# Kernel tuning notes

Measured on AMD Instinct MI355X. Metric: run time of the kernel, lower is better.

Reference implementation:

```python
import jax, jax.numpy as jnp
import numpy as np

N_NODES = 50000
N_EDGES = 800000
HIDDEN = 256
N_LAYERS = 3
N_PAIRS = 4096


def setup_inputs() -> dict:
    key = jax.random.key(0)
    ks = jax.random.split(key, 10)
    s = 1.0 / np.sqrt(HIDDEN)
    x = jax.random.normal(ks[0], (N_NODES, HIDDEN), dtype=jnp.float32)
    f0_w = jax.random.normal(ks[1], (N_LAYERS, HIDDEN, HIDDEN), dtype=jnp.float32) * s
    f0_b = jax.random.normal(ks[2], (N_LAYERS, HIDDEN), dtype=jnp.float32) * s
    f1_w = jax.random.normal(ks[3], (N_LAYERS, HIDDEN, HIDDEN), dtype=jnp.float32) * s
    f1_b = jax.random.normal(ks[4], (N_LAYERS, HIDDEN), dtype=jnp.float32) * s
    conv_w = jax.random.normal(ks[5], (N_LAYERS, HIDDEN, HIDDEN), dtype=jnp.float32) * s
    conv_b = jax.random.normal(ks[6], (N_LAYERS, HIDDEN), dtype=jnp.float32) * s
    edge_src = jax.random.randint(ks[7], (N_EDGES,), 0, N_NODES, dtype=jnp.int64 if jax.config.jax_enable_x64 else jnp.int32)
    edge_dst = jax.random.randint(ks[8], (N_EDGES,), 0, N_NODES, dtype=edge_src.dtype)
    pos = jax.random.randint(ks[9], (N_PAIRS, 2), 0, N_NODES, dtype=edge_src.dtype)
    return {"x": x, "f0_w": f0_w, "f0_b": f0_b, "f1_w": f1_w, "f1_b": f1_b,
            "conv_w": conv_w, "conv_b": conv_b,
            "edge_src": edge_src, "edge_dst": edge_dst, "pos": pos}


def reference(x, f0_w, f0_b, f1_w, f1_b, conv_w, conv_b, edge_src, edge_dst, pos):
    # Faithful translation of FLabelingNet.forward:
    #   for each layer: x0 = f0(x); x0[idx] = f1(x[idx]); x = conv(x0, adj)
    #   return x[pos]
    n = x.shape[0]
    idx = pos.reshape(-1)  # (2M,) labeled node indices
    for i in range(f0_w.shape[0]):
        x0 = x @ f0_w[i] + f0_b[i]                       # (N, F) elementwise linear
        lbl = x[idx] @ f1_w[i] + f1_b[i]                 # (2M, F) transform of labeled rows
        x0 = x0.at[idx].set(lbl)                         # scatter-overwrite selected rows
        h = x0 @ conv_w[i] + conv_b[i]                   # node-wise linear of the conv
        # sparse adjacency message passing: out[v] = sum_{(u,v) in E} h[u]
        x = jax.ops.segment_sum(h[edge_src], edge_dst, num_segments=n)
    return x[pos]  # (M, 2, F)
```

## Files before the change

### kernel.cpp

```cpp
#include <hip/hip_runtime.h>
#include <hip/hip_bf16.h>

#define N_NODES 50000
#define N_EDGES 800000
#define HIDDEN  256
#define N_LAYERS 3
#define N_PAIRS 4096
#define N_LABEL 8192
#define NPAD    50176
#define SCAN_BLOCKS (NPAD / 256)
#define WSZ (HIDDEN * HIDDEN)
#define NSTEP (HIDDEN / 32)
#define NBUCKET 196
#define EDGE_BLOCKS 196

#define NROWPAD (N_NODES + 1)
#define SLICE_ELEMS ((size_t)NROWPAD * 32)
#define SEG_CHUNKS ((N_NODES + 63) / 64)

typedef __bf16 bf16x8 __attribute__((ext_vector_type(8)));
typedef float  f32x4  __attribute__((ext_vector_type(4)));
typedef float  f32x2  __attribute__((ext_vector_type(2)));

__device__ __forceinline__ void load_lds16(const void* g, void* l) {
    __builtin_amdgcn_global_load_lds(
        (const __attribute__((address_space(1))) void*)g,
        (__attribute__((address_space(3))) void*)l, 16, 0, 0);
}

__device__ __forceinline__ void acc8(const uint4 w, f32x2* a) {
    a[0] += (f32x2){__uint_as_float(w.x << 16), __uint_as_float(w.x & 0xffff0000u)};
    a[1] += (f32x2){__uint_as_float(w.y << 16), __uint_as_float(w.y & 0xffff0000u)};
    a[2] += (f32x2){__uint_as_float(w.z << 16), __uint_as_float(w.z & 0xffff0000u)};
    a[3] += (f32x2){__uint_as_float(w.w << 16), __uint_as_float(w.w & 0xffff0000u)};
}

template <bool DEG_BIAS>
__global__ __launch_bounds__(256) void mfma_gemm_fused(
    const __bf16* __restrict__ A,
    const __bf16* __restrict__ Wt0, const __bf16* __restrict__ Wt1,
    const float* __restrict__ bD0, const float* __restrict__ bD1,
    const float* __restrict__ bC0, const float* __restrict__ bC1,
    __bf16* __restrict__ Cout,
    const int* __restrict__ idx,
    const int* __restrict__ degv,
    const int* __restrict__ flags,
    int M)
{
    const int role = blockIdx.z;
    const int bx = blockIdx.x, by = blockIdx.y;
    if (role == 1 && bx >= N_LABEL / 64) return;

    const __bf16* Wt = role ? Wt1 : Wt0;
    const float*  bD = role ? bD1 : bD0;
    const float*  bC = role ? bC1 : bC0;

    __shared__ __bf16 As[3 * 64 * 32];
    __shared__ __bf16 Bs[3 * 128 * 32];
    __shared__ int s_idx[64];

    const int t    = threadIdx.x;
    const int lane = t & 63;
    const int wave = t >> 6;
    const int m0   = bx * 64;
    const int n0   = by * 128;

    if (role == 1) {
        if (t < 64) s_idx[t] = idx[m0 + t];
        __syncthreads();
    }

    const int arow  = t >> 2;
    const int acol8 = (t & 3) * 8;
    int anode;
    if (role == 1) {
        anode = s_idx[arow];
    } else {
        const int rg = m0 + arow;
        anode = (rg < M) ? rg : (M - 1);
    }
    const __bf16* aptr = A + (size_t)anode * HIDDEN + acol8;

    const __bf16* bptr[2];
    #pragma unroll
    for (int r = 0; r < 2; ++r) {
        const int c = r * 256 + t;
        bptr[r] = Wt + (size_t)(n0 + (c >> 2)) * HIDDEN + (c & 3) * 8;
    }

    f32x4 acc[8];
    #pragma unroll
    for (int i = 0; i < 8; ++i) acc[i] = (f32x4){0.f, 0.f, 0.f, 0.f};

    const int wm   = wave * 16;
    const int fm   = lane & 15;
    const int quad = lane >> 4;

    const __bf16* bp0 = bptr[0];
    const __bf16* bp1 = bptr[1];
    #define STAGE_F(SB, K0)                                                    \
        { load_lds16(aptr + (K0), (void*)(As + (SB) * 2048 + (size_t)t * 8));  \
          load_lds16(bp0 + (K0),  (void*)(Bs + (SB) * 4096 + (size_t)t * 8));  \
          load_lds16(bp1 + (K0),  (void*)(Bs + (SB) * 4096 + (size_t)(256 + t) * 8)); }

    STAGE_F(0, 0)
    STAGE_F(1, 32)
    asm volatile("s_waitcnt vmcnt(3)" ::: "memory");
    __builtin_amdgcn_sched_barrier(0);
    __builtin_amdgcn_s_barrier();

    #pragma unroll
    for (int step = 0; step < NSTEP; ++step) {
        const int cur = step % 3;
        if (step + 2 < NSTEP) {
            const int nb = (step + 2) % 3;
            STAGE_F(nb, (step + 2) * 32)
        }
        const bf16x8 af = *(const bf16x8*)(As + cur * 2048 + (wm + fm) * 32 + quad * 8);
        bf16x8 bfr[8];
        #pragma unroll
        for (int nt = 0; nt < 8; ++nt)
            bfr[nt] = *(const bf16x8*)(Bs + cur * 4096 + (nt * 16 + fm) * 32 + quad * 8);
        #pragma unroll
        for (int nt = 0; nt < 8; ++nt)
            acc[nt] = __builtin_amdgcn_mfma_f32_16x16x32_bf16(
                af, bfr[nt], acc[nt], 0, 0, 0);
        if (step + 2 < NSTEP) asm volatile("s_waitcnt vmcnt(3)" ::: "memory");
        else                  asm volatile("s_waitcnt vmcnt(0)" ::: "memory");
        __builtin_amdgcn_sched_barrier(0);
        __builtin_amdgcn_s_barrier();
    }
    #undef STAGE_F

    float bd[8], bc[8];
    #pragma unroll
    for (int nt = 0; nt < 8; ++nt) {
        const int col = n0 + nt * 16 + fm;
        bd[nt] = DEG_BIAS ? bD[col] : 0.f;
        bc[nt] = bC[col];
    }

    #pragma unroll
    for (int rg = 0; rg < 4; ++rg) {
        const int rloc = wm + quad * 4 + rg;
        int orow;
        if (role == 1) {
            orow = s_idx[rloc];
        } else {
            orow = m0 + rloc;
            if (orow >= M) continue;
            if (flags[orow]) continue;
        }
        float bscale = 0.f;
        if constexpr (DEG_BIAS)
            bscale = (float)degv[orow];
        #pragma unroll
        for (int nt = 0; nt < 8; ++nt) {
            const int cb = n0 + nt * 16;
            float v = acc[nt][rg];
            if constexpr (DEG_BIAS) v += bscale * bd[nt];
            v += bc[nt];
            Cout[(size_t)(cb >> 5) * SLICE_ELEMS + (size_t)orow * 32
                 + (cb & 31) + fm] = (__bf16)v;
        }
    }
}

template <bool GATHER_A, bool DEG_BIAS, bool DEG_VIA_IDX, bool OUT_BF16, bool PROD_BATCH>
__global__ __launch_bounds__(256) void mfma_gemm(
    const __bf16* __restrict__ A_in,
    const __bf16* __restrict__ Wt_in,
    const float* __restrict__ biasD,
    void* __restrict__ Cout_in,
    const int* __restrict__ idx,
    const int* __restrict__ degv,
    int M)
{
    const __bf16* A  = A_in;
    const __bf16* Wt = Wt_in;
    void* Cout = Cout_in;
    if constexpr (PROD_BATCH) {
        const int z = blockIdx.z;
        A    = A_in  + (size_t)(3 * (1 + (z >> 1)) + (z & 1)) * WSZ;
        Wt   = Wt_in + (size_t)(z >> 1) * WSZ;
        Cout = (void*)((__bf16*)Cout_in + (size_t)z * WSZ);
    }

    __shared__ __bf16 As[3 * 64 * 32];
    __shared__ __bf16 Bs[3 * 128 * 32];
    __shared__ int s_idx[64];

    const int t    = threadIdx.x;
    const int lane = t & 63;
    const int wave = t >> 6;
    const int m0   = blockIdx.x * 64;
    const int n0   = blockIdx.y * 128;

    if constexpr (GATHER_A || DEG_VIA_IDX) {
        if (t < 64) s_idx[t] = idx[m0 + t];
        __syncthreads();
    }

    const int arow  = t >> 2;
    const int acol8 = (t & 3) * 8;
    int anode;
    if constexpr (GATHER_A) {
        anode = s_idx[arow];
    } else {
        const int rg = m0 + arow;
        anode = (rg < M) ? rg : (M - 1);
    }
    const __bf16* aptr = A + (size_t)anode * HIDDEN + acol8;

    const __bf16* bptr[2];
    #pragma unroll
    for (int r = 0; r < 2; ++r) {
        const int c = r * 256 + t;
        bptr[r] = Wt + (size_t)(n0 + (c >> 2)) * HIDDEN + (c & 3) * 8;
    }

    f32x4 acc[8];
    #pragma unroll
    for (int i = 0; i < 8; ++i) acc[i] = (f32x4){0.f, 0.f, 0.f, 0.f};

    const int wm   = wave * 16;
    const int fm   = lane & 15;
    const int quad = lane >> 4;

    const __bf16* bp0 = bptr[0];
    const __bf16* bp1 = bptr[1];
    #define STAGE_P(SB, K0)                                                    \
        { load_lds16(aptr + (K0), (void*)(As + (SB) * 2048 + (size_t)t * 8));  \
          load_lds16(bp0 + (K0),  (void*)(Bs + (SB) * 4096 + (size_t)t * 8));  \
          load_lds16(bp1 + (K0),  (void*)(Bs + (SB) * 4096 + (size_t)(256 + t) * 8)); }

    STAGE_P(0, 0)
    STAGE_P(1, 32)
    asm volatile("s_waitcnt vmcnt(3)" ::: "memory");
    __builtin_amdgcn_sched_barrier(0);
    __builtin_amdgcn_s_barrier();

    #pragma unroll
    for (int step = 0; step < NSTEP; ++step) {
        const int cur = step % 3;
        if (step + 2 < NSTEP) {
            const int nb = (step + 2) % 3;
            STAGE_P(nb, (step + 2) * 32)
        }
        const bf16x8 af = *(const bf16x8*)(As + cur * 2048 + (wm + fm) * 32 + quad * 8);
        bf16x8 bfr[8];
        #pragma unroll
        for (int nt = 0; nt < 8; ++nt)
            bfr[nt] = *(const bf16x8*)(Bs + cur * 4096 + (nt * 16 + fm) * 32 + quad * 8);
        #pragma unroll
        for (int nt = 0; nt < 8; ++nt)
            acc[nt] = __builtin_amdgcn_mfma_f32_16x16x32_bf16(
                af, bfr[nt], acc[nt], 0, 0, 0);
        if (step + 2 < NSTEP) asm volatile("s_waitcnt vmcnt(3)" ::: "memory");
        else                  asm volatile("s_waitcnt vmcnt(0)" ::: "memory");
        __builtin_amdgcn_sched_barrier(0);
        __builtin_amdgcn_s_barrier();
    }
    #undef STAGE_P

    float bd[8];
    #pragma unroll
    for (int nt = 0; nt < 8; ++nt)
        bd[nt] = DEG_BIAS ? biasD[n0 + nt * 16 + fm] : 0.f;

    #pragma unroll
    for (int rg = 0; rg < 4; ++rg) {
        const int rloc = wm + quad * 4 + rg;
        const int orow = m0 + rloc;
        if (!PROD_BATCH && orow >= M) continue;
        int dnode = orow;
        if constexpr (GATHER_A || DEG_VIA_IDX) dnode = s_idx[rloc];
        float bscale = 0.f;
        if constexpr (DEG_BIAS)
            bscale = (float)degv[dnode];
        #pragma unroll
        for (int nt = 0; nt < 8; ++nt) {
            const int col = n0 + nt * 16 + fm;
            float v = acc[nt][rg];
            if constexpr (DEG_BIAS) v += bscale * bd[nt];
            if constexpr (OUT_BF16)
                ((__bf16*)Cout)[(size_t)orow * HIDDEN + col] = (__bf16)v;
            else
                ((float*)Cout)[(size_t)orow * HIDDEN + col] = v;
        }
    }
}

__global__ __launch_bounds__(256) void wconv_kernel(
    const float* __restrict__ f0_w, const float* __restrict__ f1_w,
    const float* __restrict__ conv_w, const float* __restrict__ conv_b,
    __bf16* __restrict__ wt_all, __bf16* __restrict__ cw_nt,
    float* __restrict__ q,
    const int* __restrict__ edge_dst, const int* __restrict__ pos,
    int* __restrict__ blkbucket, int* __restrict__ flags,
    __bf16* __restrict__ x0b,
    const float* __restrict__ x32, __bf16* __restrict__ xb16)
{
    const int z = blockIdx.z;
    const int tx = threadIdx.x, ty = threadIdx.y;
    const int tt = ty * 32 + tx;

    if (z >= 16) {
        const int c = (z - 16) * 64 + blockIdx.x * 8 + blockIdx.y;
        const size_t base = ((size_t)c * 256 + tt) * 8;
        if (base < (size_t)N_NODES * HIDDEN) {
            const float4 u0 = *(const float4*)(x32 + base);
            const float4 u1 = *(const float4*)(x32 + base + 4);
            bf16x8 w = {(__bf16)u0.x, (__bf16)u0.y, (__bf16)u0.z, (__bf16)u0.w,
                        (__bf16)u1.x, (__bf16)u1.y, (__bf16)u1.z, (__bf16)u1.w};
            *(bf16x8*)(xb16 + base) = w;
        }
        return;
    }
    if (z >= 12) {
        __shared__ int lhist[256];
        const int blk = (z - 12) * 64 + blockIdx.x * 8 + blockIdx.y;
        if (blk >= EDGE_BLOCKS) return;
        if (blk == 0 && tt < 256) {
            const int sl = tt >> 5, c = tt & 31;
            x0b[(size_t)sl * SLICE_ELEMS + (size_t)N_NODES * 32 + c] = (__bf16)0.f;
        }
        lhist[tt] = 0;
        __syncthreads();
        const int e0 = blk * 4096;
        #pragma unroll
        for (int j = 0; j < 16; ++j) {
            const int e = e0 + j * 256 + tt;
            if (e < N_EDGES) atomicAdd(&lhist[edge_dst[e] >> 8], 1);
            if (e < N_LABEL) flags[pos[e]] = 1;
        }
        __syncthreads();
        if (tt < NBUCKET) blkbucket[blk * 256 + tt] = lhist[tt];
        return;
    }

    const int kx = blockIdx.x * 32, nx = blockIdx.y * 32;

    if (z < 9) {
        const int layer = z / 3, which = z % 3;
        const float* W = ((which == 0) ? f0_w : (which == 1) ? f1_w : conv_w)
                         + (size_t)layer * WSZ;
        __bf16* T = wt_all + (size_t)z * WSZ;

        __shared__ float tile[32][33];
        for (int i = ty; i < 32; i += 8)
            tile[i][tx] = W[(size_t)(kx + i) * HIDDEN + nx + tx];
        __syncthreads();
        for (int i = ty; i < 32; i += 8)
            T[(size_t)(nx + i) * HIDDEN + kx + tx] = (__bf16)tile[tx][i];
    } else if (z < 11) {
        const int layer = z - 9;
        const float* W = conv_w + (size_t)layer * WSZ;
        __bf16* T = cw_nt + (size_t)layer * WSZ;
        for (int i = ty; i < 32; i += 8)
            T[(size_t)(kx + i) * HIDDEN + nx + tx] =
                (__bf16)W[(size_t)(kx + i) * HIDDEN + nx + tx];
    } else {
        if (blockIdx.x >= 4 || blockIdx.y != 0) return;
        const int zq = blockIdx.x;
        const int l = zq >> 1, branch = zq & 1;
        const float* cb = conv_b + (size_t)l * HIDDEN;
        const float* W  = (branch ? f1_w : f0_w) + (size_t)(l + 1) * WSZ;
        const int n = tt;
        float s = 0.f;
        #pragma unroll 4
        for (int k = 0; k < HIDDEN; ++k)
            s += cb[k] * W[(size_t)k * HIDDEN + n];
        q[(size_t)zq * HIDDEN + n] = s;
    }
}

__device__ __forceinline__ int block_incl_scan(int v, int* s, int t)
{
    s[t] = v; __syncthreads();
    #pragma unroll
    for (int off = 1; off < 256; off <<= 1) {
        int add = (t >= off) ? s[t - off] : 0;
        __syncthreads();
        s[t] += add;
        __syncthreads();
    }
    return s[t];
}

__global__ __launch_bounds__(256) void k1b_kernel(
    const int* __restrict__ blkbucket, int* __restrict__ blkbase,
    int* __restrict__ bucket_base, int* __restrict__ bucket_size)
{
    __shared__ int s[256];
    const int t = threadIdx.x;
    int sum = 0;
    if (t < NBUCKET) {
        for (int blk = 0; blk < EDGE_BLOCKS; ++blk) {
            blkbase[blk * 256 + t] = sum;
            sum += blkbucket[blk * 256 + t];
        }
    }
    const int incl = block_incl_scan(sum, s, t);
    const int bb = incl - sum;
    if (t < NBUCKET) {
        bucket_base[t] = bb;
        bucket_size[t] = sum;
        for (int blk = 0; blk < EDGE_BLOCKS; ++blk)
            blkbase[blk * 256 + t] += bb;
    }
}

__global__ __launch_bounds__(256) void k1c_kernel(
    const int* __restrict__ esrc, const int* __restrict__ edst,
    const int* __restrict__ blkbase, unsigned int* __restrict__ bucket_buf)
{
    __shared__ int cur[256];
    const int blk = blockIdx.x;
    const int t = threadIdx.x;
    cur[t] = (t < NBUCKET) ? blkbase[blk * 256 + t] : 0;
    __syncthreads();
    const int e0 = blk * 4096;
    #pragma unroll
    for (int j = 0; j < 16; ++j) {
        const int e = e0 + j * 256 + t;
        if (e < N_EDGES) {
            const int d = edst[e];
            const int p = atomicAdd(&cur[d >> 8], 1);
            bucket_buf[p] = (unsigned int)esrc[e] | ((unsigned int)(d & 255) << 16);
        }
    }
}

__global__ __launch_bounds__(256) void k2a_kernel(
    const unsigned int* __restrict__ bucket_buf,
    const int* __restrict__ bucket_base, const int* __restrict__ bucket_size,
    int* __restrict__ counts, int* __restrict__ offs_local,
    int* __restrict__ bsum)
{
    __shared__ int lcnt[256];
    __shared__ int s[256];
    const int b = blockIdx.x;
    const int t = threadIdx.x;
    lcnt[t] = 0;
    __syncthreads();
    const int bb = bucket_base[b], sz = bucket_size[b];
    for (int j = t; j < sz; j += 256)
        atomicAdd(&lcnt[bucket_buf[bb + j] >> 16], 1);
    __syncthreads();
    const int cnt = lcnt[t];
    counts[b * 256 + t] = cnt;
    const int pv = (cnt + 7) & ~7;
    const int incl = block_incl_scan(pv, s, t);
    offs_local[b * 256 + t] = incl - pv;
    if (t == 255) bsum[b] = incl;
}

__global__ __launch_bounds__(256) void scan2_kernel(
    const int* __restrict__ bsum, int* __restrict__ bbase)
{
    __shared__ int s[256];
    const int t = threadIdx.x;
    const int v = (t < SCAN_BLOCKS) ? bsum[t] : 0;
    int incl = block_incl_scan(v, s, t);
    bbase[t] = incl - v;
}

__global__ __launch_bounds__(256) void k2b_kernel(
    const unsigned int* __restrict__ bucket_buf,
    const int* __restrict__ bucket_base, const int* __restrict__ bucket_size,
    const int* __restrict__ offs_local, const int* __restrict__ bbase,
    int* __restrict__ offs, int* __restrict__ src_sorted)
{
    __shared__ int cur[256];
    const int b = blockIdx.x;
    const int t = threadIdx.x;
    const int off = offs_local[b * 256 + t] + bbase[b];
    offs[b * 256 + t] = off;
    cur[t] = off;
    __syncthreads();
    const int bb = bucket_base[b], sz = bucket_size[b];
    for (int j = t; j < sz; j += 256) {
        const unsigned int u = bucket_buf[bb + j];
        const int p = atomicAdd(&cur[u >> 16], 1);
        src_sorted[p] = (int)(u & 0xffffu);
    }
    __syncthreads();
    const int end = cur[t];
    const int pe  = off + ((end - off + 7) & ~7);
    for (int j = end; j < pe; ++j) src_sorted[j] = N_NODES;
}

template <bool COMPACT>
__global__ __launch_bounds__(256) void seg_slice_kernel(
    const __bf16* __restrict__ x0b,
    const int* __restrict__ srcs,
    const int* __restrict__ offs,
    const int* __restrict__ nodelist,
    __bf16* __restrict__ out)
{
    const int slice = blockIdx.x & 7;
    const int chunk = blockIdx.x >> 3;
    const int t    = threadIdx.x;
    const int wave = t >> 6;
    const int lane = t & 63;
    const int g    = lane >> 2;
    const int li   = lane & 3;
    const int rw   = chunk * 64 + wave * 16 + g;
    if (!COMPACT && rw >= N_NODES) return;

    const int d    = COMPACT ? nodelist[rw] : rw;
    const int beg  = offs[d];
    const int pdeg = offs[d + 1] - beg;

    const char* xb = (const char*)(x0b + (size_t)slice * SLICE_ELEMS);
    const uint32_t lioff = (uint32_t)li * 16u;
    const int* sp = srcs + beg;

    f32x2 a[4];
    #pragma unroll
    for (int j = 0; j < 4; ++j) a[j] = (f32x2){0.f, 0.f};

    int4 j0, j1;
    if (pdeg > 0) {
        j0 = *(const int4*)(sp);
        j1 = *(const int4*)(sp + 4);
    }

    for (int base = 0; base < pdeg; base += 8) {
        const int4 k0 = j0, k1 = j1;
        if (base + 8 < pdeg) {
            j0 = *(const int4*)(sp + base + 8);
            j1 = *(const int4*)(sp + base + 12);
        }
        const uint4 c0 = *(const uint4*)(xb + (((uint32_t)k0.x << 6) + lioff));
        const uint4 c1 = *(const uint4*)(xb + (((uint32_t)k0.y << 6) + lioff));
        const uint4 c2 = *(const uint4*)(xb + (((uint32_t)k0.z << 6) + lioff));
        const uint4 c3 = *(const uint4*)(xb + (((uint32_t)k0.w << 6) + lioff));
        const uint4 c4 = *(const uint4*)(xb + (((uint32_t)k1.x << 6) + lioff));
        const uint4 c5 = *(const uint4*)(xb + (((uint32_t)k1.y << 6) + lioff));
        const uint4 c6 = *(const uint4*)(xb + (((uint32_t)k1.z << 6) + lioff));
        const uint4 c7 = *(const uint4*)(xb + (((uint32_t)k1.w << 6) + lioff));
        acc8(c0, a); acc8(c1, a); acc8(c2, a); acc8(c3, a);
        acc8(c4, a); acc8(c5, a); acc8(c6, a); acc8(c7, a);
    }

    bf16x8 o;
    #pragma unroll
    for (int j = 0; j < 4; ++j) {
        o[2 * j]     = (__bf16)a[j].x;
        o[2 * j + 1] = (__bf16)a[j].y;
    }
    *(bf16x8*)(out + (size_t)rw * HIDDEN + (slice << 5) + li * 8) = o;
}

extern "C" void kernel_launch(void* const* d_in, const int* in_sizes, int n_in,
                              void* d_out, int out_size, void* d_ws, size_t ws_size,
                              hipStream_t stream)
{
    const float* x       = (const float*)d_in[0];
    const float* f0_w    = (const float*)d_in[1];
    const float* f0_b    = (const float*)d_in[2];
    const float* f1_w    = (const float*)d_in[3];
    const float* f1_b    = (const float*)d_in[4];
    const float* conv_w  = (const float*)d_in[5];
    const float* conv_b  = (const float*)d_in[6];
    const int*   edge_src = (const int*)d_in[7];
    const int*   edge_dst = (const int*)d_in[8];
    const int*   pos      = (const int*)d_in[9];
    float* out = (float*)d_out;

    const size_t buf = (size_t)N_NODES * HIDDEN;

    char* p = (char*)d_ws;
    __bf16* bufA   = (__bf16*)p; p += buf * 2;
    __bf16* bufB   = (__bf16*)p; p += SLICE_ELEMS * 8 * 2;
    __bf16* s_lbl  = (__bf16*)p; p += (size_t)N_LABEL * HIDDEN * 2;
    __bf16* wt_all = (__bf16*)p; p += (size_t)9 * WSZ * 2;
    __bf16* prod   = (__bf16*)p; p += (size_t)4 * WSZ * 2;
    __bf16* cw_nt  = (__bf16*)p; p += (size_t)2 * WSZ * 2;
    float*  qv     = (float*)p;  p += (size_t)4 * HIDDEN * 4;
    int* flags      = (int*)p;  p += NPAD * 4;
    int* counts     = (int*)p;  p += NPAD * 4;
    int* offs_local = (int*)p;  p += NPAD * 4;
    int* offs       = (int*)p;  p += NPAD * 4;
    int* bsum       = (int*)p;  p += 256 * 4;
    int* bbase      = (int*)p;  p += 256 * 4;
    int* blkbucket  = (int*)p;  p += (size_t)EDGE_BLOCKS * 256 * 4;
    int* blkbase    = (int*)p;  p += (size_t)EDGE_BLOCKS * 256 * 4;
    int* bucket_base= (int*)p;  p += 256 * 4;
    int* bucket_size= (int*)p;  p += 256 * 4;
    unsigned int* bucket_buf = (unsigned int*)p; p += (size_t)N_EDGES * 4;
    int* src_sorted = (int*)p;  p += (size_t)(N_EDGES + 7 * NPAD) * 4;

    hipMemsetAsync(flags, 0, NPAD * sizeof(int), stream);
    wconv_kernel<<<dim3(8, 8, 114), dim3(32, 8), 0, stream>>>(
        f0_w, f1_w, conv_w, conv_b, wt_all, cw_nt, qv,
        edge_dst, pos, blkbucket, flags, bufB, x, bufA);
    k1b_kernel<<<1, 256, 0, stream>>>(blkbucket, blkbase, bucket_base, bucket_size);
    k1c_kernel<<<EDGE_BLOCKS, 256, 0, stream>>>(edge_src, edge_dst, blkbase, bucket_buf);
    k2a_kernel<<<NBUCKET, 256, 0, stream>>>(
        bucket_buf, bucket_base, bucket_size, counts, offs_local, bsum);
    scan2_kernel<<<1, 256, 0, stream>>>(bsum, bbase);
    k2b_kernel<<<NBUCKET, 256, 0, stream>>>(
        bucket_buf, bucket_base, bucket_size, offs_local, bbase, offs, src_sorted);

    mfma_gemm<false, false, false, true, true><<<dim3(4, 2, 4), 256, 0, stream>>>(
        wt_all, cw_nt, nullptr, prod, nullptr, nullptr, HIDDEN);

    const dim3 fused_grid(782, 2, 2);
    const dim3 lbl_grid(128, 2);

    __bf16* cur = bufA;
    __bf16* tmp = bufB;

    for (int l = 0; l < N_LAYERS; ++l) {
        const float* B0 = f0_b + (size_t)l * HIDDEN;
        const float* B1 = f1_b + (size_t)l * HIDDEN;

        if (l == 0) {
            mfma_gemm_fused<false><<<fused_grid, 256, 0, stream>>>(
                bufA, wt_all + 0 * WSZ, wt_all + 1 * WSZ,
                nullptr, nullptr, B0, B1, tmp, pos, counts, flags, N_NODES);
        } else {
            const int z0 = (l - 1) * 2;
            mfma_gemm_fused<true><<<fused_grid, 256, 0, stream>>>(
                cur, prod + (size_t)z0 * WSZ, prod + (size_t)(z0 + 1) * WSZ,
                qv + (size_t)z0 * HIDDEN, qv + (size_t)(z0 + 1) * HIDDEN,
                B0, B1, tmp, pos, counts, flags, N_NODES);
        }

        if (l < N_LAYERS - 1) {
            seg_slice_kernel<false><<<8 * SEG_CHUNKS, 256, 0, stream>>>(
                tmp, src_sorted, offs, nullptr, cur);
        } else {
            seg_slice_kernel<true><<<8 * (N_LABEL / 64), 256, 0, stream>>>(
                tmp, src_sorted, offs, pos, s_lbl);
            mfma_gemm<false, true, true, false, false><<<lbl_grid, 256, 0, stream>>>(
                s_lbl, wt_all + (size_t)(2 * 3 + 2) * WSZ,
                conv_b + (size_t)2 * HIDDEN, out, pos, counts, N_LABEL);
        }
    }
}
```

Baseline: 370.4 us.

## Parallelize bucket offset scan and store sorted sources as 16-bit indices

Replaces the single-block serial loop over 196 edge blocks per bucket with a 196-block kernel that scans each bucket column in parallel, followed by a tiny scan of bucket sizes; k1c now adds the bucket base when it loads. The sorted source indices move from 32-bit to 16-bit storage, which halves the index traffic in the gather kernel that runs every layer, and one 16-byte load now yields 8 indices. This relies on node ids fitting in 16 bits (N_NODES = 50000 < 65536) and adds one more kernel launch.

```diff
diff --git a/kernel.cpp b/kernel.cpp
--- a/kernel.cpp
+++ b/kernel.cpp
@@ -388,37 +388,38 @@
     return s[t];
 }
 
-__global__ __launch_bounds__(256) void k1b_kernel(
+__global__ __launch_bounds__(256) void k1b1_kernel(
     const int* __restrict__ blkbucket, int* __restrict__ blkbase,
-    int* __restrict__ bucket_base, int* __restrict__ bucket_size)
+    int* __restrict__ bucket_size)
+{
+    __shared__ int s[256];
+    const int b = blockIdx.x;
+    const int t = threadIdx.x;
+    const int v = (t < EDGE_BLOCKS) ? blkbucket[t * 256 + b] : 0;
+    const int incl = block_incl_scan(v, s, t);
+    if (t < EDGE_BLOCKS) blkbase[t * 256 + b] = incl - v;
+    if (t == 255) bucket_size[b] = incl;
+}
+
+__global__ __launch_bounds__(256) void k1b2_kernel(
+    const int* __restrict__ bucket_size, int* __restrict__ bucket_base)
 {
     __shared__ int s[256];
     const int t = threadIdx.x;
-    int sum = 0;
-    if (t < NBUCKET) {
-        for (int blk = 0; blk < EDGE_BLOCKS; ++blk) {
-            blkbase[blk * 256 + t] = sum;
-            sum += blkbucket[blk * 256 + t];
-        }
-    }
-    const int incl = block_incl_scan(sum, s, t);
-    const int bb = incl - sum;
-    if (t < NBUCKET) {
-        bucket_base[t] = bb;
-        bucket_size[t] = sum;
-        for (int blk = 0; blk < EDGE_BLOCKS; ++blk)
-            blkbase[blk * 256 + t] += bb;
-    }
+    const int v = (t < NBUCKET) ? bucket_size[t] : 0;
+    const int incl = block_incl_scan(v, s, t);
+    if (t < NBUCKET) bucket_base[t] = incl - v;
 }
 
 __global__ __launch_bounds__(256) void k1c_kernel(
     const int* __restrict__ esrc, const int* __restrict__ edst,
-    const int* __restrict__ blkbase, unsigned int* __restrict__ bucket_buf)
+    const int* __restrict__ blkbase, const int* __restrict__ bucket_base,
+    unsigned int* __restrict__ bucket_buf)
 {
     __shared__ int cur[256];
     const int blk = blockIdx.x;
     const int t = threadIdx.x;
-    cur[t] = (t < NBUCKET) ? blkbase[blk * 256 + t] : 0;
+    cur[t] = (t < NBUCKET) ? blkbase[blk * 256 + t] + bucket_base[t] : 0;
     __syncthreads();
     const int e0 = blk * 4096;
     #pragma unroll
@@ -470,7 +471,7 @@
     const unsigned int* __restrict__ bucket_buf,
     const int* __restrict__ bucket_base, const int* __restrict__ bucket_size,
     const int* __restrict__ offs_local, const int* __restrict__ bbase,
-    int* __restrict__ offs, int* __restrict__ src_sorted)
+    int* __restrict__ offs, unsigned short* __restrict__ src_sorted)
 {
     __shared__ int cur[256];
     const int b = blockIdx.x;
@@ -483,18 +484,18 @@
     for (int j = t; j < sz; j += 256) {
         const unsigned int u = bucket_buf[bb + j];
         const int p = atomicAdd(&cur[u >> 16], 1);
-        src_sorted[p] = (int)(u & 0xffffu);
+        src_sorted[p] = (unsigned short)(u & 0xffffu);
     }
     __syncthreads();
     const int end = cur[t];
     const int pe  = off + ((end - off + 7) & ~7);
-    for (int j = end; j < pe; ++j) src_sorted[j] = N_NODES;
+    for (int j = end; j < pe; ++j) src_sorted[j] = (unsigned short)N_NODES;
 }
 
 template <bool COMPACT>
 __global__ __launch_bounds__(256) void seg_slice_kernel(
     const __bf16* __restrict__ x0b,
-    const int* __restrict__ srcs,
+    const unsigned short* __restrict__ srcs,
     const int* __restrict__ offs,
     const int* __restrict__ nodelist,
     __bf16* __restrict__ out)
@@ -515,32 +516,31 @@
 
     const char* xb = (const char*)(x0b + (size_t)slice * SLICE_ELEMS);
     const uint32_t lioff = (uint32_t)li * 16u;
-    const int* sp = srcs + beg;
+    const unsigned short* sp = srcs + beg;
 
     f32x2 a[4];
     #pragma unroll
     for (int j = 0; j < 4; ++j) a[j] = (f32x2){0.f, 0.f};
 
-    int4 j0, j1;
-    if (pdeg > 0) {
-        j0 = *(const int4*)(sp);
-        j1 = *(const int4*)(sp + 4);
-    }
+    uint4 j0;
+    if (pdeg > 0) j0 = *(const uint4*)(sp);
 
     for (int base = 0; base < pdeg; base += 8) {
-        const int4 k0 = j0, k1 = j1;
-        if (base + 8 < pdeg) {
-            j0 = *(const int4*)(sp + base + 8);
-            j1 = *(const int4*)(sp + base + 12);
-        }
-        const uint4 c0 = *(const uint4*)(xb + (((uint32_t)k0.x << 6) + lioff));
-        const uint4 c1 = *(const uint4*)(xb + (((uint32_t)k0.y << 6) + lioff));
-        const uint4 c2 = *(const uint4*)(xb + (((uint32_t)k0.z << 6) + lioff));
-        const uint4 c3 = *(const uint4*)(xb + (((uint32_t)k0.w << 6) + lioff));
-        const uint4 c4 = *(const uint4*)(xb + (((uint32_t)k1.x << 6) + lioff));
-        const uint4 c5 = *(const uint4*)(xb + (((uint32_t)k1.y << 6) + lioff));
-        const uint4 c6 = *(const uint4*)(xb + (((uint32_t)k1.z << 6) + lioff));
-        const uint4 c7 = *(const uint4*)(xb + (((uint32_t)k1.w << 6) + lioff));
+        const uint4 kv = j0;
+        if (base + 8 < pdeg)
+            j0 = *(const uint4*)(sp + base + 8);
+        const uint32_t i0 = kv.x & 0xffffu, i1 = kv.x >> 16;
+        const uint32_t i2 = kv.y & 0xffffu, i3 = kv.y >> 16;
+        const uint32_t i4 = kv.z & 0xffffu, i5 = kv.z >> 16;
+        const uint32_t i6 = kv.w & 0xffffu, i7 = kv.w >> 16;
+        const uint4 c0 = *(const uint4*)(xb + ((i0 << 6) + lioff));
+        const uint4 c1 = *(const uint4*)(xb + ((i1 << 6) + lioff));
+        const uint4 c2 = *(const uint4*)(xb + ((i2 << 6) + lioff));
+        const uint4 c3 = *(const uint4*)(xb + ((i3 << 6) + lioff));
+        const uint4 c4 = *(const uint4*)(xb + ((i4 << 6) + lioff));
+        const uint4 c5 = *(const uint4*)(xb + ((i5 << 6) + lioff));
+        const uint4 c6 = *(const uint4*)(xb + ((i6 << 6) + lioff));
+        const uint4 c7 = *(const uint4*)(xb + ((i7 << 6) + lioff));
         acc8(c0, a); acc8(c1, a); acc8(c2, a); acc8(c3, a);
         acc8(c4, a); acc8(c5, a); acc8(c6, a); acc8(c7, a);
     }
@@ -591,14 +591,17 @@
     int* bucket_base= (int*)p;  p += 256 * 4;
     int* bucket_size= (int*)p;  p += 256 * 4;
     unsigned int* bucket_buf = (unsigned int*)p; p += (size_t)N_EDGES * 4;
-    int* src_sorted = (int*)p;  p += (size_t)(N_EDGES + 7 * NPAD) * 4;
+    unsigned short* src_sorted = (unsigned short*)p;
+    p += (((size_t)(N_EDGES + 7 * NPAD) * 2 + 15) & ~(size_t)15);
 
     hipMemsetAsync(flags, 0, NPAD * sizeof(int), stream);
     wconv_kernel<<<dim3(8, 8, 114), dim3(32, 8), 0, stream>>>(
         f0_w, f1_w, conv_w, conv_b, wt_all, cw_nt, qv,
         edge_dst, pos, blkbucket, flags, bufB, x, bufA);
-    k1b_kernel<<<1, 256, 0, stream>>>(blkbucket, blkbase, bucket_base, bucket_size);
-    k1c_kernel<<<EDGE_BLOCKS, 256, 0, stream>>>(edge_src, edge_dst, blkbase, bucket_buf);
+    k1b1_kernel<<<NBUCKET, 256, 0, stream>>>(blkbucket, blkbase, bucket_size);
+    k1b2_kernel<<<1, 256, 0, stream>>>(bucket_size, bucket_base);
+    k1c_kernel<<<EDGE_BLOCKS, 256, 0, stream>>>(
+        edge_src, edge_dst, blkbase, bucket_base, bucket_buf);
     k2a_kernel<<<NBUCKET, 256, 0, stream>>>(
         bucket_buf, bucket_base, bucket_size, counts, offs_local, bsum);
     scan2_kernel<<<1, 256, 0, stream>>>(bsum, bbase);
```

Result: faster. 329.1 us (-11.2%).
